# Optimization experiments

Measured on AMD Instinct MI355X. Metric: run time of the kernel, lower is better.

The kernel has to match this reference:

```python
import jax, jax.numpy as jnp
import numpy as np

N_NODE = 50000
N_EDGE = 800000
NODE_DIM, EDGE_DIM = 3, 4


def _relu(x):
    return jnp.maximum(x, 0)


def setup_inputs() -> dict:
    key = jax.random.key(0)
    ks = jax.random.split(key, 32)
    ki = iter(range(32))

    def w(shape):
        fan = shape[0]
        return (jax.random.normal(ks[next(ki)], shape, jnp.float32) / np.float32(np.sqrt(fan)))

    def b(n):
        return jnp.zeros((n,), jnp.float32)

    inp = {
        'nodes': jax.random.normal(ks[next(ki)], (N_NODE, NODE_DIM), jnp.float32),
        'edges': jax.random.normal(ks[next(ki)], (N_EDGE, EDGE_DIM), jnp.float32),
        'senders': jax.random.randint(ks[next(ki)], (N_EDGE,), 0, N_NODE, jnp.int32),
        'receivers': jax.random.randint(ks[next(ki)], (N_EDGE,), 0, N_NODE, jnp.int32),
        # psi1 encoder: [10 -> 256 -> 256 -> 128], relu after every layer (act_final=True)
        'mw0': w((NODE_DIM * 2 + EDGE_DIM, 256)), 'mb0': b(256),
        'mw1': w((256, 256)), 'mb1': b(256),
        'mw2': w((256, 128)), 'mb2': b(128),
        # psi2 attention: [128 -> 128 -> 128 -> 1], no final act
        'aw0': w((128, 128)), 'ab0': b(128),
        'aw1': w((128, 128)), 'ab1': b(128),
        'aw2': w((128, 1)), 'ab2': b(1),
        # psi3 value: [128 -> 256 -> 128], relu after every layer
        'vw0': w((128, 256)), 'vb0': b(256),
        'vw1': w((256, 128)), 'vb1': b(128),
        # psi4 decoder: [128 -> 256 -> 256 -> 1], no final act
        'uw0': w((128, 256)), 'ub0': b(256),
        'uw1': w((256, 256)), 'ub1': b(256),
        'uw2': w((256, 1)), 'ub2': b(1),
    }
    return inp


def reference(nodes, edges, senders, receivers,
              mw0, mb0, mw1, mb1, mw2, mb2,
              aw0, ab0, aw1, ab1, aw2, ab2,
              vw0, vb0, vw1, vb1,
              uw0, ub0, uw1, ub1, uw2, ub2):
    n_node = nodes.shape[0]
    # gather endpoint features and concat with edge features: (E, 2*node_dim+edge_dim)
    z = jnp.concatenate([nodes[senders], nodes[receivers], edges], axis=-1)
    # psi1 encoder (act_final=True)
    q = _relu(_relu(_relu(z @ mw0 + mb0) @ mw1 + mb1) @ mw2 + mb2)  # (E,128)
    # psi2 attention logits (no final act)
    w = (_relu(_relu(q @ aw0 + ab0) @ aw1 + ab1) @ aw2 + ab2)[:, 0]  # (E,)
    # segment softmax over receivers (matches torch scatter_reduce amax with -1e9 init)
    m = jax.ops.segment_max(w, receivers, num_segments=n_node)
    m = jnp.maximum(m, jnp.float32(-1e9))
    ex = jnp.exp(w - m[receivers])
    s = jax.ops.segment_sum(ex, receivers, num_segments=n_node)
    attn = ex / (s[receivers] + 1e-12)  # (E,)
    # psi3 value (act_final=True)
    v = _relu(_relu(q @ vw0 + vb0) @ vw1 + vb1)  # (E,128)
    # attention-weighted scatter-add aggregation to receiver nodes
    aggr = jax.ops.segment_sum(attn[:, None] * v, receivers, num_segments=n_node)  # (N,128)
    # psi4 decoder (no final act)
    out = _relu(_relu(aggr @ uw0 + ub0) @ uw1 + ub1) @ uw2 + ub2  # (N,1)
    return out
```

## Files before the change

### kernel.cpp

```cpp
#include <hip/hip_runtime.h>
#include <stdint.h>

#define NN_NODE 50000
#define NN_EDGE 800000

typedef _Float16 f16;
typedef _Float16 f16x2 __attribute__((ext_vector_type(2)));
typedef _Float16 f16x8 __attribute__((ext_vector_type(8)));
typedef float f32x4 __attribute__((ext_vector_type(4)));

#define WT_MW0   0
#define WT_MW1   8192
#define WT_MW2   73728
#define WT_AW0   106496
#define WT_AW1   122880
#define WT_VW0   139264
#define WT_VW1   172032
#define WT_UW0   204800
#define WT_UW1   237568
#define WT_TOTAL 303104

#define V_OFF      606208ull
#define WL_OFF     205406208ull
#define CNT_OFF    208606208ull
#define BASE_OFF   208806208ull
#define AGGR_OFF   209006208ull

__device__ __forceinline__ int swz(int row, int col) {
    return row * 256 + ((((col >> 3) ^ (row & 7))) << 3) + (col & 7);
}

template<int K, int N>
__device__ __forceinline__ void mfma_layer(const f16* in, int inoff,
        const f16* __restrict__ wt, const float* __restrict__ bias,
        f16* out, int outoff, int tid)
{
    const int wave = tid >> 6;
    const int lane = tid & 63;
    const int l15  = lane & 15;
    const int quad = lane >> 4;
    constexpr int NCT = N >> 4;
    constexpr int NKS = K >> 5;
    for (int ct = wave; ct < NCT; ct += 4) {
        const int n = ct * 16 + l15;
        f16x8 bf[NKS];
        const f16* wrow = wt + (size_t)n * K + quad * 8;
#pragma unroll
        for (int ks = 0; ks < NKS; ++ks) bf[ks] = *(const f16x8*)(wrow + ks * 32);
        const float bv = bias[n];
#pragma unroll
        for (int ms = 0; ms < 4; ++ms) {
            f32x4 acc = {0.f, 0.f, 0.f, 0.f};
            const int arow = ms * 16 + l15;
#pragma unroll
            for (int ks = 0; ks < NKS; ++ks) {
                const int acol = inoff + ks * 32 + quad * 8;
                const f16x8 af = *(const f16x8*)(in + swz(arow, acol));
                acc = __builtin_amdgcn_mfma_f32_16x16x32_f16(af, bf[ks], acc, 0, 0, 0);
            }
            const int orow0 = ms * 16 + quad * 4;
#pragma unroll
            for (int i = 0; i < 4; ++i) {
                float y = acc[i] + bv;
                y = fmaxf(y, 0.f);
                out[swz(orow0 + i, outoff + ct * 16 + l15)] = (f16)y;
            }
        }
    }
}

struct WSeg { const float* src; int K, N, Kpad, dstOff; };
struct WSegs { WSeg s[9]; };

__global__ void prep_kernel(WSegs segs, f16* __restrict__ wt) {
    int idx = blockIdx.x * 256 + threadIdx.x;
    if (idx >= WT_TOTAL) return;
    int off = idx;
#pragma unroll
    for (int i = 0; i < 9; ++i) {
        int sz = segs.s[i].N * segs.s[i].Kpad;
        if (off < sz) {
            int n = off / segs.s[i].Kpad;
            int k = off - n * segs.s[i].Kpad;
            f16 val = (f16)0.f;
            if (k < segs.s[i].K) val = (f16)segs.s[i].src[k * segs.s[i].N + n];
            wt[segs.s[i].dstOff + off] = val;
            return;
        }
        off -= sz;
    }
}

__global__ void hist_kernel(const int* __restrict__ receivers, int* __restrict__ cnt) {
    int e = blockIdx.x * 256 + threadIdx.x;
    atomicAdd(&cnt[receivers[e]], 1);
}

__global__ __launch_bounds__(1024) void scan_kernel(int* __restrict__ cnt, int* __restrict__ base) {
    __shared__ int psum[1024];
    const int tid = threadIdx.x;
    const int CH = (NN_NODE + 1023) / 1024;
    const int lo = tid * CH;
    const int hi = min(lo + CH, NN_NODE);
    int s = 0;
    for (int i = lo; i < hi; ++i) s += cnt[i];
    psum[tid] = s;
    __syncthreads();
    for (int d = 1; d < 1024; d <<= 1) {
        int v = (tid >= d) ? psum[tid - d] : 0;
        __syncthreads();
        psum[tid] += v;
        __syncthreads();
    }
    int run = psum[tid] - s;
    for (int i = lo; i < hi; ++i) {
        int c = cnt[i];
        base[i] = run;
        cnt[i] = run;
        run += c;
    }
}

__global__ __launch_bounds__(256, 2) void edge_kernel(
        const float* __restrict__ nodes, const float* __restrict__ edges,
        const int* __restrict__ senders, const int* __restrict__ receivers,
        const f16* __restrict__ wt,
        const float* __restrict__ mb0, const float* __restrict__ mb1, const float* __restrict__ mb2,
        const float* __restrict__ ab0, const float* __restrict__ ab1,
        const float* __restrict__ aw2, const float* __restrict__ ab2,
        const float* __restrict__ vb0, const float* __restrict__ vb1,
        f16* __restrict__ vout, float* __restrict__ wlog, int* __restrict__ cursor)
{
    __shared__ f16 ldsbuf[2 * 64 * 256];
    __shared__ int spos[64];
    f16* bufA = ldsbuf;
    f16* bufB = ldsbuf + 64 * 256;
    const int tid = threadIdx.x;
    const int e0 = blockIdx.x * 64;

    {
        int e = tid & 63, part = tid >> 6;
        if (part == 0) {
            int s = senders[e0 + e];
            for (int c = 0; c < 3; ++c) bufA[swz(e, c)] = (f16)nodes[s * 3 + c];
        } else if (part == 1) {
            int r = receivers[e0 + e];
            for (int c = 0; c < 3; ++c) bufA[swz(e, 3 + c)] = (f16)nodes[r * 3 + c];
        } else if (part == 2) {
            const float4 ev = *(const float4*)(edges + (size_t)(e0 + e) * 4);
            bufA[swz(e, 6)] = (f16)ev.x; bufA[swz(e, 7)] = (f16)ev.y;
            bufA[swz(e, 8)] = (f16)ev.z; bufA[swz(e, 9)] = (f16)ev.w;
        } else {
            for (int c = 10; c < 32; ++c) bufA[swz(e, c)] = (f16)0.f;
        }
    }
    __syncthreads();

    mfma_layer< 32, 256>(bufA, 0, wt + WT_MW0, mb0, bufB, 0, tid); __syncthreads();
    mfma_layer<256, 256>(bufB, 0, wt + WT_MW1, mb1, bufA, 0, tid); __syncthreads();
    mfma_layer<256, 128>(bufA, 0, wt + WT_MW2, mb2, bufB, 0, tid); __syncthreads();
    mfma_layer<128, 128>(bufB, 0, wt + WT_AW0, ab0, bufA, 0, tid); __syncthreads();
    mfma_layer<128, 128>(bufA, 0, wt + WT_AW1, ab1, bufA, 128, tid); __syncthreads();

    {
        int e = tid >> 2, part = tid & 3;
        float sum = 0.f;
        for (int c = part * 32; c < part * 32 + 32; ++c)
            sum += (float)bufA[swz(e, 128 + c)] * aw2[c];
        sum += __shfl_down(sum, 2);
        sum += __shfl_down(sum, 1);
        if (part == 0) {
            float wv = sum + ab2[0];
            int r = receivers[e0 + e];
            int pos = atomicAdd(&cursor[r], 1);
            spos[e] = pos;
            wlog[pos] = wv;
        }
    }
    __syncthreads();

    mfma_layer<128, 256>(bufB, 0, wt + WT_VW0, vb0, bufA, 0, tid); __syncthreads();
    mfma_layer<256, 128>(bufA, 0, wt + WT_VW1, vb1, bufB, 0, tid); __syncthreads();

    {
        int row = tid >> 2, j = tid & 3;
        uint4* dst = (uint4*)(vout + (size_t)spos[row] * 128);
#pragma unroll
        for (int i = 0; i < 4; ++i) {
            int chunk = j * 4 + i;
            const uint4 val = *(const uint4*)(bufB + row * 256 + ((chunk ^ (row & 7)) * 8));
            dst[chunk] = val;
        }
    }
}

__global__ __launch_bounds__(256) void aggregate_kernel(
        const float* __restrict__ wlog, const f16* __restrict__ v,
        const int* __restrict__ base, float* __restrict__ aggr)
{
    const int tid = threadIdx.x;
    const int n = blockIdx.x * 4 + (tid >> 6);
    const int lane = tid & 63;
    const int st = base[n];
    const int en = (n == NN_NODE - 1) ? NN_EDGE : base[n + 1];

    float mx = -1e9f;
    for (int i = st + lane; i < en; i += 64) mx = fmaxf(mx, wlog[i]);
#pragma unroll
    for (int d = 1; d < 64; d <<= 1) mx = fmaxf(mx, __shfl_xor(mx, d));

    float sm = 0.f;
    for (int i = st + lane; i < en; i += 64) sm += __expf(wlog[i] - mx);
#pragma unroll
    for (int d = 1; d < 64; d <<= 1) sm += __shfl_xor(sm, d);
    const float inv = 1.f / (sm + 1e-12f);

    float acc0 = 0.f, acc1 = 0.f;
    const f16* vp = v + (size_t)st * 128 + lane * 2;
    for (int i = st; i < en; ++i, vp += 128) {
        float attn = __expf(wlog[i] - mx) * inv;
        f16x2 vv = *(const f16x2*)vp;
        acc0 += attn * (float)vv[0];
        acc1 += attn * (float)vv[1];
    }
    float2 o; o.x = acc0; o.y = acc1;
    *(float2*)(aggr + (size_t)n * 128 + lane * 2) = o;
}

__global__ __launch_bounds__(256, 2) void node_kernel(
        const float* __restrict__ aggr, const f16* __restrict__ wt,
        const float* __restrict__ ub0, const float* __restrict__ ub1,
        const float* __restrict__ uw2, const float* __restrict__ ub2,
        float* __restrict__ out)
{
    __shared__ f16 ldsbuf[2 * 64 * 256];
    f16* bufA = ldsbuf;
    f16* bufB = ldsbuf + 64 * 256;
    const int tid = threadIdx.x;
    const int n0 = blockIdx.x * 64;
    {
        int row = tid >> 2, j = tid & 3;
        int n = n0 + row;
        if (n < NN_NODE) {
            const float4* src = (const float4*)(aggr + (size_t)n * 128 + j * 32);
#pragma unroll
            for (int i = 0; i < 8; ++i) {
                float4 t4 = src[i];
                int c = j * 32 + i * 4;
                bufA[swz(row, c + 0)] = (f16)t4.x;
                bufA[swz(row, c + 1)] = (f16)t4.y;
                bufA[swz(row, c + 2)] = (f16)t4.z;
                bufA[swz(row, c + 3)] = (f16)t4.w;
            }
        } else {
#pragma unroll
            for (int i = 0; i < 32; ++i) bufA[swz(row, j * 32 + i)] = (f16)0.f;
        }
    }
    __syncthreads();
    mfma_layer<128, 256>(bufA, 0, wt + WT_UW0, ub0, bufB, 0, tid); __syncthreads();
    mfma_layer<256, 256>(bufB, 0, wt + WT_UW1, ub1, bufA, 0, tid); __syncthreads();
    {
        int e = tid >> 2, part = tid & 3;
        float sum = 0.f;
        for (int c = part * 64; c < part * 64 + 64; ++c)
            sum += (float)bufA[swz(e, c)] * uw2[c];
        sum += __shfl_down(sum, 2);
        sum += __shfl_down(sum, 1);
        int n = n0 + e;
        if (part == 0 && n < NN_NODE) out[n] = sum + ub2[0];
    }
}

extern "C" void kernel_launch(void* const* d_in, const int* in_sizes, int n_in,
                              void* d_out, int out_size, void* d_ws, size_t ws_size,
                              hipStream_t stream)
{
    const float* nodes     = (const float*)d_in[0];
    const float* edges     = (const float*)d_in[1];
    const int*   senders   = (const int*)d_in[2];
    const int*   receivers = (const int*)d_in[3];
    const float* mw0 = (const float*)d_in[4];  const float* mb0 = (const float*)d_in[5];
    const float* mw1 = (const float*)d_in[6];  const float* mb1 = (const float*)d_in[7];
    const float* mw2 = (const float*)d_in[8];  const float* mb2 = (const float*)d_in[9];
    const float* aw0 = (const float*)d_in[10]; const float* ab0 = (const float*)d_in[11];
    const float* aw1 = (const float*)d_in[12]; const float* ab1 = (const float*)d_in[13];
    const float* aw2 = (const float*)d_in[14]; const float* ab2 = (const float*)d_in[15];
    const float* vw0 = (const float*)d_in[16]; const float* vb0 = (const float*)d_in[17];
    const float* vw1 = (const float*)d_in[18]; const float* vb1 = (const float*)d_in[19];
    const float* uw0 = (const float*)d_in[20]; const float* ub0 = (const float*)d_in[21];
    const float* uw1 = (const float*)d_in[22]; const float* ub1 = (const float*)d_in[23];
    const float* uw2 = (const float*)d_in[24]; const float* ub2 = (const float*)d_in[25];

    char* ws = (char*)d_ws;
    f16*   wt   = (f16*)ws;
    f16*   vbuf = (f16*)(ws + V_OFF);
    float* wlog = (float*)(ws + WL_OFF);
    int*   cnt  = (int*)(ws + CNT_OFF);
    int*   base = (int*)(ws + BASE_OFF);
    float* aggr = (float*)(ws + AGGR_OFF);
    float* out  = (float*)d_out;

    hipMemsetAsync(cnt, 0, NN_NODE * sizeof(int), stream);

    WSegs segs = {{
        { mw0,  10, 256,  32, WT_MW0 },
        { mw1, 256, 256, 256, WT_MW1 },
        { mw2, 256, 128, 256, WT_MW2 },
        { aw0, 128, 128, 128, WT_AW0 },
        { aw1, 128, 128, 128, WT_AW1 },
        { vw0, 128, 256, 128, WT_VW0 },
        { vw1, 256, 128, 256, WT_VW1 },
        { uw0, 128, 256, 128, WT_UW0 },
        { uw1, 256, 256, 256, WT_UW1 },
    }};
    prep_kernel<<<(WT_TOTAL + 255) / 256, 256, 0, stream>>>(segs, wt);

    hist_kernel<<<NN_EDGE / 256, 256, 0, stream>>>(receivers, cnt);
    scan_kernel<<<1, 1024, 0, stream>>>(cnt, base);

    edge_kernel<<<NN_EDGE / 64, 256, 0, stream>>>(nodes, edges, senders, receivers, wt,
        mb0, mb1, mb2, ab0, ab1, aw2, ab2, vb0, vb1, vbuf, wlog, cnt);

    aggregate_kernel<<<NN_NODE / 4, 256, 0, stream>>>(wlog, vbuf, base, aggr);

    node_kernel<<<(NN_NODE + 63) / 64, 256, 0, stream>>>(aggr, wt, ub0, ub1, uw2, ub2, out);
}
```

Measured before the change: 1.055 ms.

## Switch MLP layers to 32x32x16 MFMA with 32-row blocks and higher occupancy

Replaces the 16x16x32 MFMA layer routine with a 32x32x16 variant. Edge and node tiles shrink from 64 to 32 rows so LDS use halves and the launch bound allows 4 blocks per CU. The goal is fewer MFMA issues and better latency hiding. In exchange, each weight tile loaded into registers is reused over half as many rows, so weight traffic per edge roughly doubles.

```diff
diff --git a/kernel.cpp b/kernel.cpp
--- a/kernel.cpp
+++ b/kernel.cpp
@@ -8,6 +8,7 @@
 typedef _Float16 f16x2 __attribute__((ext_vector_type(2)));
 typedef _Float16 f16x8 __attribute__((ext_vector_type(8)));
 typedef float f32x4 __attribute__((ext_vector_type(4)));
+typedef float f32x16 __attribute__((ext_vector_type(16)));
 
 #define WT_MW0   0
 #define WT_MW1   8192
@@ -31,40 +32,36 @@
 }
 
 template<int K, int N>
-__device__ __forceinline__ void mfma_layer(const f16* in, int inoff,
+__device__ __forceinline__ void mfma_layer32(const f16* in, int inoff,
         const f16* __restrict__ wt, const float* __restrict__ bias,
         f16* out, int outoff, int tid)
 {
     const int wave = tid >> 6;
     const int lane = tid & 63;
-    const int l15  = lane & 15;
-    const int quad = lane >> 4;
-    constexpr int NCT = N >> 4;
-    constexpr int NKS = K >> 5;
+    const int l31  = lane & 31;
+    const int kh   = lane >> 5;
+    constexpr int NCT = N >> 5;
+    constexpr int NKS = K >> 4;
+#pragma unroll 1
     for (int ct = wave; ct < NCT; ct += 4) {
-        const int n = ct * 16 + l15;
+        const int n = ct * 32 + l31;
+        const f16* wrow = wt + (size_t)n * K + kh * 8;
         f16x8 bf[NKS];
-        const f16* wrow = wt + (size_t)n * K + quad * 8;
-#pragma unroll
-        for (int ks = 0; ks < NKS; ++ks) bf[ks] = *(const f16x8*)(wrow + ks * 32);
+#pragma unroll
+        for (int ks = 0; ks < NKS; ++ks) bf[ks] = *(const f16x8*)(wrow + ks * 16);
         const float bv = bias[n];
-#pragma unroll
-        for (int ms = 0; ms < 4; ++ms) {
-            f32x4 acc = {0.f, 0.f, 0.f, 0.f};
-            const int arow = ms * 16 + l15;
-#pragma unroll
-            for (int ks = 0; ks < NKS; ++ks) {
-                const int acol = inoff + ks * 32 + quad * 8;
-                const f16x8 af = *(const f16x8*)(in + swz(arow, acol));
-                acc = __builtin_amdgcn_mfma_f32_16x16x32_f16(af, bf[ks], acc, 0, 0, 0);
-            }
-            const int orow0 = ms * 16 + quad * 4;
-#pragma unroll
-            for (int i = 0; i < 4; ++i) {
-                float y = acc[i] + bv;
-                y = fmaxf(y, 0.f);
-                out[swz(orow0 + i, outoff + ct * 16 + l15)] = (f16)y;
-            }
+        f32x16 acc = {0.f,0.f,0.f,0.f,0.f,0.f,0.f,0.f,0.f,0.f,0.f,0.f,0.f,0.f,0.f,0.f};
+#pragma unroll
+        for (int ks = 0; ks < NKS; ++ks) {
+            const f16x8 af = *(const f16x8*)(in + swz(l31, inoff + ks * 16 + kh * 8));
+            acc = __builtin_amdgcn_mfma_f32_32x32x16_f16(af, bf[ks], acc, 0, 0, 0);
+        }
+#pragma unroll
+        for (int reg = 0; reg < 16; ++reg) {
+            const int row = (reg & 3) + 8 * (reg >> 2) + 4 * kh;
+            float y = acc[reg] + bv;
+            y = fmaxf(y, 0.f);
+            out[swz(row, outoff + n)] = (f16)y;
         }
     }
 }
@@ -121,7 +118,7 @@
     }
 }
 
-__global__ __launch_bounds__(256, 2) void edge_kernel(
+__global__ __launch_bounds__(256, 4) void edge_kernel(
         const float* __restrict__ nodes, const float* __restrict__ edges,
         const int* __restrict__ senders, const int* __restrict__ receivers,
         const f16* __restrict__ wt,
@@ -131,15 +128,15 @@
         const float* __restrict__ vb0, const float* __restrict__ vb1,
         f16* __restrict__ vout, float* __restrict__ wlog, int* __restrict__ cursor)
 {
-    __shared__ f16 ldsbuf[2 * 64 * 256];
-    __shared__ int spos[64];
+    __shared__ f16 ldsbuf[2 * 32 * 256];
+    __shared__ int spos[32];
     f16* bufA = ldsbuf;
-    f16* bufB = ldsbuf + 64 * 256;
+    f16* bufB = ldsbuf + 32 * 256;
     const int tid = threadIdx.x;
-    const int e0 = blockIdx.x * 64;
-
-    {
-        int e = tid & 63, part = tid >> 6;
+    const int e0 = blockIdx.x * 32;
+
+    {
+        int e = tid & 31, part = tid >> 5;
         if (part == 0) {
             int s = senders[e0 + e];
             for (int c = 0; c < 3; ++c) bufA[swz(e, c)] = (f16)nodes[s * 3 + c];
@@ -150,23 +147,24 @@
             const float4 ev = *(const float4*)(edges + (size_t)(e0 + e) * 4);
             bufA[swz(e, 6)] = (f16)ev.x; bufA[swz(e, 7)] = (f16)ev.y;
             bufA[swz(e, 8)] = (f16)ev.z; bufA[swz(e, 9)] = (f16)ev.w;
-        } else {
+        } else if (part == 3) {
             for (int c = 10; c < 32; ++c) bufA[swz(e, c)] = (f16)0.f;
         }
     }
     __syncthreads();
 
-    mfma_layer< 32, 256>(bufA, 0, wt + WT_MW0, mb0, bufB, 0, tid); __syncthreads();
-    mfma_layer<256, 256>(bufB, 0, wt + WT_MW1, mb1, bufA, 0, tid); __syncthreads();
-    mfma_layer<256, 128>(bufA, 0, wt + WT_MW2, mb2, bufB, 0, tid); __syncthreads();
-    mfma_layer<128, 128>(bufB, 0, wt + WT_AW0, ab0, bufA, 0, tid); __syncthreads();
-    mfma_layer<128, 128>(bufA, 0, wt + WT_AW1, ab1, bufA, 128, tid); __syncthreads();
-
-    {
-        int e = tid >> 2, part = tid & 3;
+    mfma_layer32< 32, 256>(bufA, 0, wt + WT_MW0, mb0, bufB, 0, tid); __syncthreads();
+    mfma_layer32<256, 256>(bufB, 0, wt + WT_MW1, mb1, bufA, 0, tid); __syncthreads();
+    mfma_layer32<256, 128>(bufA, 0, wt + WT_MW2, mb2, bufB, 0, tid); __syncthreads();
+    mfma_layer32<128, 128>(bufB, 0, wt + WT_AW0, ab0, bufA, 0, tid); __syncthreads();
+    mfma_layer32<128, 128>(bufA, 0, wt + WT_AW1, ab1, bufA, 128, tid); __syncthreads();
+
+    {
+        int e = tid >> 3, part = tid & 7;
         float sum = 0.f;
-        for (int c = part * 32; c < part * 32 + 32; ++c)
+        for (int c = part * 16; c < part * 16 + 16; ++c)
             sum += (float)bufA[swz(e, 128 + c)] * aw2[c];
+        sum += __shfl_down(sum, 4);
         sum += __shfl_down(sum, 2);
         sum += __shfl_down(sum, 1);
         if (part == 0) {
@@ -179,15 +177,15 @@
     }
     __syncthreads();
 
-    mfma_layer<128, 256>(bufB, 0, wt + WT_VW0, vb0, bufA, 0, tid); __syncthreads();
-    mfma_layer<256, 128>(bufA, 0, wt + WT_VW1, vb1, bufB, 0, tid); __syncthreads();
-
-    {
-        int row = tid >> 2, j = tid & 3;
+    mfma_layer32<128, 256>(bufB, 0, wt + WT_VW0, vb0, bufA, 0, tid); __syncthreads();
+    mfma_layer32<256, 128>(bufA, 0, wt + WT_VW1, vb1, bufB, 0, tid); __syncthreads();
+
+    {
+        int row = tid >> 3, j = tid & 7;
         uint4* dst = (uint4*)(vout + (size_t)spos[row] * 128);
 #pragma unroll
-        for (int i = 0; i < 4; ++i) {
-            int chunk = j * 4 + i;
+        for (int i = 0; i < 2; ++i) {
+            int chunk = j * 2 + i;
             const uint4 val = *(const uint4*)(bufB + row * 256 + ((chunk ^ (row & 7)) * 8));
             dst[chunk] = val;
         }
@@ -227,26 +225,26 @@
     *(float2*)(aggr + (size_t)n * 128 + lane * 2) = o;
 }
 
-__global__ __launch_bounds__(256, 2) void node_kernel(
+__global__ __launch_bounds__(256, 4) void node_kernel(
         const float* __restrict__ aggr, const f16* __restrict__ wt,
         const float* __restrict__ ub0, const float* __restrict__ ub1,
         const float* __restrict__ uw2, const float* __restrict__ ub2,
         float* __restrict__ out)
 {
-    __shared__ f16 ldsbuf[2 * 64 * 256];
+    __shared__ f16 ldsbuf[2 * 32 * 256];
     f16* bufA = ldsbuf;
-    f16* bufB = ldsbuf + 64 * 256;
+    f16* bufB = ldsbuf + 32 * 256;
     const int tid = threadIdx.x;
-    const int n0 = blockIdx.x * 64;
-    {
-        int row = tid >> 2, j = tid & 3;
+    const int n0 = blockIdx.x * 32;
+    {
+        int row = tid >> 3, j = tid & 7;
         int n = n0 + row;
         if (n < NN_NODE) {
-            const float4* src = (const float4*)(aggr + (size_t)n * 128 + j * 32);
-#pragma unroll
-            for (int i = 0; i < 8; ++i) {
+            const float4* src = (const float4*)(aggr + (size_t)n * 128 + j * 16);
+#pragma unroll
+            for (int i = 0; i < 4; ++i) {
                 float4 t4 = src[i];
-                int c = j * 32 + i * 4;
+                int c = j * 16 + i * 4;
                 bufA[swz(row, c + 0)] = (f16)t4.x;
                 bufA[swz(row, c + 1)] = (f16)t4.y;
                 bufA[swz(row, c + 2)] = (f16)t4.z;
@@ -254,17 +252,18 @@
             }
         } else {
 #pragma unroll
-            for (int i = 0; i < 32; ++i) bufA[swz(row, j * 32 + i)] = (f16)0.f;
+            for (int i = 0; i < 16; ++i) bufA[swz(row, j * 16 + i)] = (f16)0.f;
         }
     }
     __syncthreads();
-    mfma_layer<128, 256>(bufA, 0, wt + WT_UW0, ub0, bufB, 0, tid); __syncthreads();
-    mfma_layer<256, 256>(bufB, 0, wt + WT_UW1, ub1, bufA, 0, tid); __syncthreads();
-    {
-        int e = tid >> 2, part = tid & 3;
+    mfma_layer32<128, 256>(bufA, 0, wt + WT_UW0, ub0, bufB, 0, tid); __syncthreads();
+    mfma_layer32<256, 256>(bufB, 0, wt + WT_UW1, ub1, bufA, 0, tid); __syncthreads();
+    {
+        int e = tid >> 3, part = tid & 7;
         float sum = 0.f;
-        for (int c = part * 64; c < part * 64 + 64; ++c)
+        for (int c = part * 32; c < part * 32 + 32; ++c)
             sum += (float)bufA[swz(e, c)] * uw2[c];
+        sum += __shfl_down(sum, 4);
         sum += __shfl_down(sum, 2);
         sum += __shfl_down(sum, 1);
         int n = n0 + e;
@@ -319,10 +318,10 @@
     hist_kernel<<<NN_EDGE / 256, 256, 0, stream>>>(receivers, cnt);
     scan_kernel<<<1, 1024, 0, stream>>>(cnt, base);
 
-    edge_kernel<<<NN_EDGE / 64, 256, 0, stream>>>(nodes, edges, senders, receivers, wt,
+    edge_kernel<<<NN_EDGE / 32, 256, 0, stream>>>(nodes, edges, senders, receivers, wt,
         mb0, mb1, mb2, ab0, ab1, aw2, ab2, vb0, vb1, vbuf, wlog, cnt);
 
     aggregate_kernel<<<NN_NODE / 4, 256, 0, stream>>>(wlog, vbuf, base, aggr);
 
-    node_kernel<<<(NN_NODE + 63) / 64, 256, 0, stream>>>(aggr, wt, ub0, ub1, uw2, ub2, out);
-}
+    node_kernel<<<(NN_NODE + 31) / 32, 256, 0, stream>>>(aggr, wt, ub0, ub1, uw2, ub2, out);
+}
```

Measured after the change: 1.489 ms. 41.1% more time.

## Hoist activation fragments into registers and swap MFMA operands for vector stores

Applied to the files above, without the earlier changes.

Activation fragments for all four row tiles are loaded from LDS once per wave and kept in registers, instead of being reloaded for every output column tile. The MFMA operands are swapped so each lane's accumulator holds four consecutive output features of one row. That allows a single 8-byte vectorized store and a float4 bias load in place of four scalar strided LDS writes. The cost is higher register pressure (4*NKS f16x8 registers, up to 32 VGPR quads for K=256), which may lower occupancy.

```diff
diff --git a/kernel.cpp b/kernel.cpp
--- a/kernel.cpp
+++ b/kernel.cpp
@@ -6,6 +6,7 @@
 
 typedef _Float16 f16;
 typedef _Float16 f16x2 __attribute__((ext_vector_type(2)));
+typedef _Float16 f16x4 __attribute__((ext_vector_type(4)));
 typedef _Float16 f16x8 __attribute__((ext_vector_type(8)));
 typedef float f32x4 __attribute__((ext_vector_type(4)));
 
@@ -41,30 +42,34 @@
     const int quad = lane >> 4;
     constexpr int NCT = N >> 4;
     constexpr int NKS = K >> 5;
+
+    f16x8 af[4][NKS];
+#pragma unroll
+    for (int ms = 0; ms < 4; ++ms)
+#pragma unroll
+        for (int ks = 0; ks < NKS; ++ks)
+            af[ms][ks] = *(const f16x8*)(in + swz(ms * 16 + l15, inoff + ks * 32 + quad * 8));
+
+#pragma unroll 1
     for (int ct = wave; ct < NCT; ct += 4) {
-        const int n = ct * 16 + l15;
         f16x8 bf[NKS];
-        const f16* wrow = wt + (size_t)n * K + quad * 8;
+        const f16* wrow = wt + (size_t)(ct * 16 + l15) * K + quad * 8;
 #pragma unroll
         for (int ks = 0; ks < NKS; ++ks) bf[ks] = *(const f16x8*)(wrow + ks * 32);
-        const float bv = bias[n];
+        const int f0 = ct * 16 + quad * 4;
+        const float4 bv = *(const float4*)(bias + f0);
 #pragma unroll
         for (int ms = 0; ms < 4; ++ms) {
             f32x4 acc = {0.f, 0.f, 0.f, 0.f};
-            const int arow = ms * 16 + l15;
-#pragma unroll
-            for (int ks = 0; ks < NKS; ++ks) {
-                const int acol = inoff + ks * 32 + quad * 8;
-                const f16x8 af = *(const f16x8*)(in + swz(arow, acol));
-                acc = __builtin_amdgcn_mfma_f32_16x16x32_f16(af, bf[ks], acc, 0, 0, 0);
-            }
-            const int orow0 = ms * 16 + quad * 4;
-#pragma unroll
-            for (int i = 0; i < 4; ++i) {
-                float y = acc[i] + bv;
-                y = fmaxf(y, 0.f);
-                out[swz(orow0 + i, outoff + ct * 16 + l15)] = (f16)y;
-            }
+#pragma unroll
+            for (int ks = 0; ks < NKS; ++ks)
+                acc = __builtin_amdgcn_mfma_f32_16x16x32_f16(bf[ks], af[ms][ks], acc, 0, 0, 0);
+            f16x4 o;
+            o[0] = (f16)fmaxf(acc[0] + bv.x, 0.f);
+            o[1] = (f16)fmaxf(acc[1] + bv.y, 0.f);
+            o[2] = (f16)fmaxf(acc[2] + bv.z, 0.f);
+            o[3] = (f16)fmaxf(acc[3] + bv.w, 0.f);
+            *(f16x4*)(out + swz(ms * 16 + l15, outoff + f0)) = o;
         }
     }
 }
```

After: 1.073 ms. Within noise of the previous version (+1.7%).
